# Kernel tuning notes

Measured on AMD Instinct MI355X. Metric: run time of the kernel, lower is better.

## Reference

```python
import jax, jax.numpy as jnp
import numpy as np
from jax import lax

B, N, D = 8, 16384, 64
NPOINT, NSAMPLE, RADIUS = 1024, 32, 0.1
MLP = [3 + D, 64, 64, 128]
BN_EPS = 1e-5


def setup_inputs() -> dict:
    key = jax.random.key(0)
    ks = jax.random.split(key, 8)
    inp = {
        'xyz': jax.random.uniform(ks[0], (B, 3, N), dtype=jnp.float32),
        'points': jax.random.normal(ks[1], (B, D, N), dtype=jnp.float32),
    }
    for i, (cin, cout) in enumerate(zip(MLP[:-1], MLP[1:]), start=1):
        inp[f'w{i}'] = jax.random.normal(ks[1 + i], (cout, cin), dtype=jnp.float32) / np.sqrt(cin)
        inp[f'b{i}'] = jnp.zeros((cout,), jnp.float32)
        inp[f'g{i}'] = jnp.ones((cout,), jnp.float32)
        inp[f'be{i}'] = jnp.zeros((cout,), jnp.float32)
    return inp


def farthest_point_sample(xyz, npoint):
    # xyz: (B, N, 3). Deterministic start at index 0 (torch uses randint).
    b, n, _ = xyz.shape

    def step(carry, _):
        distance, farthest = carry  # (B,N), (B,)
        centroid = jnp.take_along_axis(xyz, farthest[:, None, None], axis=1)  # (B,1,3)
        dist = jnp.sum((xyz - centroid) ** 2, axis=-1)  # (B,N)
        distance = jnp.minimum(distance, dist)
        new_far = jnp.argmax(distance, axis=-1).astype(jnp.int32)
        return (distance, new_far), farthest

    init = (jnp.full((b, n), 1e10, xyz.dtype), jnp.zeros((b,), jnp.int32))
    _, idxs = lax.scan(step, init, None, length=npoint)  # (npoint, B)
    return idxs.T  # (B, npoint)


def query_ball_point(radius, nsample, xyz, new_xyz):
    # xyz: (B,N,3), new_xyz: (B,S,3) -> (B,S,nsample) int32
    b, n, _ = xyz.shape
    # squared pairwise distances (B,S,N)
    sqr = (jnp.sum(new_xyz ** 2, -1)[:, :, None]
           + jnp.sum(xyz ** 2, -1)[:, None, :]
           - 2.0 * jnp.einsum('bsc,bnc->bsn', new_xyz, xyz))
    group_idx = jnp.where(sqr > radius ** 2, n, jnp.arange(n, dtype=jnp.int32))
    group_idx = jnp.sort(group_idx, axis=-1)[:, :, :nsample]
    first = group_idx[:, :, :1]
    return jnp.where(group_idx == n, first, group_idx)


def reference(xyz, points, w1, b1, g1, be1, w2, b2, g2, be2, w3, b3, g3, be3):
    xyz_t = xyz.transpose(0, 2, 1)      # (B,N,3)
    pts_t = points.transpose(0, 2, 1)   # (B,N,D)
    bsz = xyz_t.shape[0]

    fps_idx = farthest_point_sample(xyz_t, NPOINT)          # (B,S)
    bidx2 = jnp.arange(bsz)[:, None]
    new_xyz = xyz_t[bidx2, fps_idx]                          # (B,S,3)

    idx = query_ball_point(RADIUS, NSAMPLE, xyz_t, new_xyz)  # (B,S,ns)
    bidx3 = jnp.arange(bsz)[:, None, None]
    grouped_xyz = xyz_t[bidx3, idx] - new_xyz[:, :, None, :]  # (B,S,ns,3)
    grouped_pts = pts_t[bidx3, idx]                           # (B,S,ns,D)
    feat = jnp.concatenate([grouped_xyz, grouped_pts], axis=-1)  # (B,S,ns,C)

    for w, b, g, be in ((w1, b1, g1, be1), (w2, b2, g2, be2), (w3, b3, g3, be3)):
        feat = jnp.einsum('bsnc,oc->bsno', feat, w) + b
        mean = feat.mean(axis=(0, 1, 2))
        var = feat.var(axis=(0, 1, 2))  # biased, as torch BN uses for normalization
        feat = (feat - mean) * lax.rsqrt(var + BN_EPS) * g + be
        feat = jax.nn.relu(feat)

    new_points = feat.max(axis=2)  # max over nsample -> (B,S,Cout)
    return new_xyz.transpose(0, 2, 1), new_points.transpose(0, 2, 1)
```

## Files before the change

kernel.cpp:

```cpp
#include <hip/hip_runtime.h>
#include <hip/hip_bf16.h>
#include <stdint.h>

#define BATCH 8
#define NPTS  16384
#define DIMF  64
#define SPTS  1024
#define NSAMP 32
#define MTOT  (BATCH*SPTS*NSAMP)
#define CELLS 512

__device__ __forceinline__ float bfu_lo(uint32_t u){ return __uint_as_float(u<<16); }
__device__ __forceinline__ float bfu_hi(uint32_t u){ return __uint_as_float(u & 0xffff0000u); }
__device__ __forceinline__ uint16_t f2bf(float f){
  __hip_bfloat16 h = __float2bfloat16(f);
  uint16_t u; __builtin_memcpy(&u, &h, 2); return u;
}

__device__ __forceinline__ unsigned long long shfl_xor_u64(unsigned long long v, int off){
  unsigned lo = (unsigned)v, hi = (unsigned)(v>>32);
  lo = __shfl_xor(lo, off); hi = __shfl_xor(hi, off);
  return ((unsigned long long)hi<<32) | lo;
}

__global__ __launch_bounds__(256) void transpose_kernel(const float* __restrict__ pts,
                                                        float* __restrict__ ptsT){
  __shared__ float tile[32][33];
  int b = blockIdx.z;
  int n0 = blockIdx.x*32, c0 = blockIdx.y*32;
  int tx = threadIdx.x & 31, ty = threadIdx.x >> 5;
  const float* src = pts + (size_t)b*DIMF*NPTS;
  float* dst = ptsT + (size_t)b*NPTS*DIMF;
#pragma unroll
  for (int j=0;j<4;j++)
    tile[ty+8*j][tx] = src[(size_t)(c0+ty+8*j)*NPTS + n0 + tx];
  __syncthreads();
#pragma unroll
  for (int j=0;j<4;j++)
    dst[(size_t)(n0+ty+8*j)*DIMF + c0 + tx] = tile[tx][ty+8*j];
}

__device__ __forceinline__ int cell_of(float x, float y, float z){
  int ix=(int)(x*8.0f); ix = ix<0?0:(ix>7?7:ix);
  int iy=(int)(y*8.0f); iy = iy<0?0:(iy>7?7:iy);
  int iz=(int)(z*8.0f); iz = iz<0?0:(iz>7?7:iz);
  return (ix<<6)|(iy<<3)|iz;
}

__global__ __launch_bounds__(512) void fps_kernel(const float* __restrict__ xyz,
                                                  float* __restrict__ out0,
                                                  float4* __restrict__ sortg){
  int b = blockIdx.x;
  const float* X = xyz + (size_t)b*3*NPTS;
  float4* sp = sortg + (size_t)b*NPTS;
  int t = threadIdx.x, lane = t & 63, w = t >> 6;

  __shared__ float dst_s[NPTS];
  __shared__ int   hist[CELLS];
  __shared__ int   cursor[CELLS];
  __shared__ int   cstart[CELLS+1];
  __shared__ float cmaxv[CELLS];
  __shared__ int   cmaxk[CELLS];
  __shared__ float cwx[CELLS], cwy[CELLS], cwz[CELLS];
  __shared__ int   wsum[8];
  __shared__ float4 pf4[2][8];
  __shared__ unsigned long long pk64[2][8];

  if (t < CELLS) hist[t] = 0;
  __syncthreads();
#pragma unroll
  for (int k=0;k<32;k++){
    int n = t + (k<<9);
    atomicAdd(&hist[cell_of(X[n],X[NPTS+n],X[2*NPTS+n])],1);
  }
  __syncthreads();
  {
    int v = hist[t], inc = v;
#pragma unroll
    for (int off=1; off<64; off<<=1){ int u=__shfl_up(inc,off); if(lane>=off) inc+=u; }
    if (lane==63) wsum[w] = inc;
    __syncthreads();
    if (t==0){ int acc=0; for(int i=0;i<8;i++){int x=wsum[i]; wsum[i]=acc; acc+=x;} }
    __syncthreads();
    int ex = inc - v + wsum[w];
    cstart[t]=ex; cursor[t]=ex;
    cmaxv[t] = (v>0)?1e10f:0.0f;
    cmaxk[t] = 16383;
    if (t==0) cstart[CELLS]=NPTS;
  }
  __syncthreads();
#pragma unroll
  for (int k=0;k<32;k++){
    int n = t + (k<<9);
    float x=X[n], y=X[NPTS+n], z=X[2*NPTS+n];
    int c = cell_of(x,y,z);
    int pos = atomicAdd(&cursor[c],1);
    sp[pos] = make_float4(x,y,z,__int_as_float(n));
  }
  for (int n=t;n<NPTS;n+=512) dst_s[n]=1e10f;
  __syncthreads();

  int ix = (((lane>>5)&1)<<2) | (((lane>>4)&1)<<1) | ((w>>2)&1);
  int iy = (((lane>>3)&1)<<2) | (((lane>>2)&1)<<1) | ((w>>1)&1);
  int iz = (((lane>>1)&1)<<2) | (( lane    &1)<<1) | ( w    &1);
  int cm = (ix<<6)|(iy<<3)|iz;
  float lox=ix*0.125f, loy=iy*0.125f, loz=iz*0.125f;

  float cx=X[0], cy=X[NPTS], cz=X[2*NPTS];
  float* o = out0 + (size_t)b*3*SPTS;
  for (int s=0;s<SPTS;s++){
    if (t==0){ o[s]=cx; o[SPTS+s]=cy; o[2*SPTS+s]=cz; }
    if (s==SPTS-1) break;
    float dxx = fmaxf(fmaxf(lox-cx, cx-(lox+0.125f)),0.f);
    float dyy = fmaxf(fmaxf(loy-cy, cy-(loy+0.125f)),0.f);
    float dzz = fmaxf(fmaxf(loz-cz, cz-(loz+0.125f)),0.f);
    float lb = dxx*dxx+dyy*dyy+dzz*dzz;
    bool dirty = (lb*(1.0f-4e-6f)-4e-6f) < cmaxv[cm];
    unsigned long long mask = __ballot(dirty);
    while (mask){
      int l = (int)__builtin_ctzll(mask); mask &= mask-1;
      int jx = (((l>>5)&1)<<2) | (((l>>4)&1)<<1) | ((w>>2)&1);
      int jy = (((l>>3)&1)<<2) | (((l>>2)&1)<<1) | ((w>>1)&1);
      int jz = (((l>>1)&1)<<2) | (( l    &1)<<1) | ( w    &1);
      int c = (jx<<6)|(jy<<3)|jz;
      int st = cstart[c], en = cstart[c+1];
      if (st >= en) continue;
      unsigned long long bp = 0ull; float bd=0.f,bx=0.f,by=0.f,bz=0.f;
      for (int base=st; base<en; base+=64){
        int pos = base+lane;
        if (pos<en){
          float4 pq = sp[pos];
          float ddx=__fsub_rn(pq.x,cx), ddy=__fsub_rn(pq.y,cy), ddz=__fsub_rn(pq.z,cz);
          float d = __fadd_rn(__fadd_rn(__fmul_rn(ddx,ddx),__fmul_rn(ddy,ddy)),
                              __fmul_rn(ddz,ddz));
          float od = dst_s[pos];
          d = fminf(od, d);
          dst_s[pos] = d;
          int orig = __float_as_int(pq.w);
          unsigned long long pk =
            ((unsigned long long)__float_as_uint(d)<<32) | (unsigned)(16383-orig);
          if (pk > bp){ bp=pk; bd=d; bx=pq.x; by=pq.y; bz=pq.z; }
        }
      }
      unsigned long long rp = bp;
#pragma unroll
      for (int off=1; off<64; off<<=1){
        unsigned long long op = shfl_xor_u64(rp, off);
        rp = (op>rp)? op : rp;
      }
      unsigned long long wm = __ballot(bp==rp);
      int wl = (int)__builtin_ctzll(wm);
      if (lane==wl){
        cmaxv[c]=bd;
        cmaxk[c]=16383-(int)(bp & 0xffffffffull);
        cwx[c]=bx; cwy[c]=by; cwz[c]=bz;
      }
    }
    __builtin_amdgcn_wave_barrier();
    int p = s & 1;
    {
      float v = cmaxv[cm]; int kk = cmaxk[cm];
      unsigned long long p2 =
        ((unsigned long long)__float_as_uint(v)<<32) | (unsigned)(16383-kk);
      unsigned long long r2 = p2;
#pragma unroll
      for (int off=1; off<64; off<<=1){
        unsigned long long o2 = shfl_xor_u64(r2, off);
        r2 = (o2>r2)? o2 : r2;
      }
      unsigned long long wm2 = __ballot(p2==r2);
      int wl2 = (int)__builtin_ctzll(wm2);
      if (lane==wl2){
        pf4[p][w] = make_float4(cwx[cm], cwy[cm], cwz[cm], 0.f);
        pk64[p][w] = r2;
      }
    }
    __syncthreads();
    {
      unsigned long long fv = pk64[p][lane&7], fr = fv;
#pragma unroll
      for (int off=1; off<8; off<<=1){
        unsigned long long of = shfl_xor_u64(fr, off);
        fr = (of>fr)? of : fr;
      }
      unsigned long long fm = __ballot(fv==fr);
      int fl = (int)__builtin_ctzll(fm) & 7;
      float4 cc = pf4[p][fl];
      cx=cc.x; cy=cc.y; cz=cc.z;
    }
  }
}

__global__ __launch_bounds__(256) void ball_kernel(const float* __restrict__ xyz,
                                                   const float* __restrict__ newxyz,
                                                   int* __restrict__ idxo){
  int b  = blockIdx.x >> 5;
  int sc = blockIdx.x & 31;
  const float* X  = xyz + (size_t)b*3*NPTS;
  int t = threadIdx.x, lane = t & 63, w = t >> 6;
  __shared__ float lx[512], ly[512], lz[512], ls[512];
  __shared__ int done;
  if (t==0) done = 0;
  const float rsq = 0.01f;
  float nx[8], ny[8], nz[8], sn[8];
  int cnt[8], first[8];
  int sbase = sc*32 + w*8;
#pragma unroll
  for (int q=0;q<8;q++){
    int s = sbase + q;
    nx[q] = newxyz[(size_t)b*3*SPTS + s];
    ny[q] = newxyz[(size_t)b*3*SPTS + SPTS + s];
    nz[q] = newxyz[(size_t)b*3*SPTS + 2*SPTS + s];
    sn[q] = __fadd_rn(__fadd_rn(__fmul_rn(nx[q],nx[q]),__fmul_rn(ny[q],ny[q])),
                      __fmul_rn(nz[q],nz[q]));
    cnt[q]=0; first[q]=0;
  }
  __syncthreads();
  for (int T=0;T<32;T++){
    {
      float ax = X[T*512 + t], ay = X[NPTS + T*512 + t], az = X[2*NPTS + T*512 + t];
      lx[t]=ax; ly[t]=ay; lz[t]=az;
      ls[t] = __fadd_rn(__fadd_rn(__fmul_rn(ax,ax),__fmul_rn(ay,ay)),__fmul_rn(az,az));
      float bx = X[T*512 + t + 256], by = X[NPTS + T*512 + t + 256], bz = X[2*NPTS + T*512 + t + 256];
      lx[t+256]=bx; ly[t+256]=by; lz[t+256]=bz;
      ls[t+256] = __fadd_rn(__fadd_rn(__fmul_rn(bx,bx),__fmul_rn(by,by)),__fmul_rn(bz,bz));
    }
    __syncthreads();
#pragma unroll
    for (int q=0;q<8;q++){
      if (cnt[q] >= NSAMP) continue;
      int s = sbase + q;
      int* op = idxo + ((size_t)(b*SPTS + s))*NSAMP;
      for (int c=0;c<8;c++){
        int li = c*64 + lane;
        float dot = fmaf(nz[q], lz[li], fmaf(ny[q], ly[li], __fmul_rn(nx[q], lx[li])));
        float sq  = __fsub_rn(__fadd_rn(sn[q], ls[li]), __fmul_rn(2.0f, dot));
        bool in = (sq <= rsq);
        unsigned long long m = __ballot(in);
        if (cnt[q]==0 && m) first[q] = T*512 + c*64 + (int)__builtin_ctzll(m);
        if (in){
          int slot = cnt[q] + (int)__popcll(m & ((1ull<<lane)-1ull));
          if (slot < NSAMP) op[slot] = T*512 + li;
        }
        cnt[q] += (int)__popcll(m);
        if (cnt[q] >= NSAMP){ if (lane==0) atomicAdd(&done,1); break; }
      }
    }
    __syncthreads();
    if (done >= 32) break;
  }
#pragma unroll
  for (int q=0;q<8;q++){
    if (cnt[q] < NSAMP){
      int s = sbase + q;
      int* op = idxo + ((size_t)(b*SPTS + s))*NSAMP;
      if (lane >= cnt[q] && lane < NSAMP) op[lane] = first[q];
    }
  }
}

__global__ __launch_bounds__(256) void gemm1_kernel(const float* __restrict__ xyz,
                                                    const float* __restrict__ ptsT,
                                                    const int* __restrict__ idx,
                                                    const float* __restrict__ newxyz,
                                                    const float* __restrict__ w1,
                                                    const float* __restrict__ b1,
                                                    uint16_t* __restrict__ y1){
  __shared__ float As[128*69];
  __shared__ float Ws[67*64];
  __shared__ float bias[64];
  __shared__ int   ndx[128];
  __shared__ float nxs[4][3];
  int t = threadIdx.x;
  int g0 = blockIdx.x*128;
  if (t < 128) ndx[t] = idx[g0 + t];
  if (t < 12){
    int grp = t/3, c = t%3;
    int bs = (g0>>5) + grp; int b = bs>>10, s = bs & 1023;
    nxs[grp][c] = newxyz[(size_t)b*3*SPTS + c*SPTS + s];
  }
  if (t < 64) bias[t] = b1[t];
  for (int e=t; e<67*64; e+=256){ int k=e>>6, c=e&63; Ws[k*64+c] = w1[c*67+k]; }
  __syncthreads();
  {
    int r = t>>1, h = t&1;
    int n = ndx[r];
    int bs = (g0>>5) + (r>>5); int b = bs>>10;
    const float* pr = ptsT + ((size_t)(b*NPTS + n))*64 + h*32;
    float* ar = As + r*69;
    if (h==0){
      int grp = r>>5;
      ar[0] = __fsub_rn(xyz[(size_t)b*3*NPTS + n],          nxs[grp][0]);
      ar[1] = __fsub_rn(xyz[(size_t)b*3*NPTS + NPTS + n],   nxs[grp][1]);
      ar[2] = __fsub_rn(xyz[(size_t)b*3*NPTS + 2*NPTS + n], nxs[grp][2]);
    }
    float* ap = ar + 3 + h*32;
#pragma unroll
    for (int j=0;j<8;j++){
      float4 v = *(const float4*)(pr + j*4);
      ap[j*4+0]=v.x; ap[j*4+1]=v.y; ap[j*4+2]=v.z; ap[j*4+3]=v.w;
    }
  }
  __syncthreads();
  int rg = t>>3, cg = t&7;
  float acc[4][8];
#pragma unroll
  for (int i=0;i<4;i++)
#pragma unroll
    for (int j=0;j<8;j++) acc[i][j]=0.f;
  for (int k=0;k<67;k++){
    float a0 = As[(rg*4+0)*69+k];
    float a1 = As[(rg*4+1)*69+k];
    float a2 = As[(rg*4+2)*69+k];
    float a3 = As[(rg*4+3)*69+k];
    const float* wr = Ws + k*64 + cg*8;
    float4 w0 = *(const float4*)wr;
    float4 w1v = *(const float4*)(wr+4);
    float wj[8] = {w0.x,w0.y,w0.z,w0.w,w1v.x,w1v.y,w1v.z,w1v.w};
#pragma unroll
    for (int j=0;j<8;j++){
      acc[0][j] = fmaf(a0, wj[j], acc[0][j]);
      acc[1][j] = fmaf(a1, wj[j], acc[1][j]);
      acc[2][j] = fmaf(a2, wj[j], acc[2][j]);
      acc[3][j] = fmaf(a3, wj[j], acc[3][j]);
    }
  }
#pragma unroll
  for (int i=0;i<4;i++){
    int gr = g0 + rg*4 + i;
    uint16_t* yr = y1 + (size_t)gr*64 + cg*8;
    uint4 vv;
    uint32_t u[4];
#pragma unroll
    for (int j=0;j<4;j++){
      float v0 = acc[i][2*j]   + bias[cg*8+2*j];
      float v1 = acc[i][2*j+1] + bias[cg*8+2*j+1];
      u[j] = (uint32_t)f2bf(v0) | ((uint32_t)f2bf(v1)<<16);
    }
    vv.x=u[0]; vv.y=u[1]; vv.z=u[2]; vv.w=u[3];
    *(uint4*)yr = vv;
  }
}

__global__ __launch_bounds__(256) void gemm2_kernel(const uint16_t* __restrict__ yin,
                                                    const float* __restrict__ w2,
                                                    const float* __restrict__ b2,
                                                    const float* __restrict__ scale,
                                                    const float* __restrict__ shift,
                                                    uint16_t* __restrict__ yout){
  __shared__ float As[128*65];
  __shared__ float Ws[64*64];
  __shared__ float bias[64], sc[64], sh[64];
  int t = threadIdx.x;
  int g0 = blockIdx.x*128;
  if (t < 64){ bias[t]=b2[t]; sc[t]=scale[t]; sh[t]=shift[t]; }
  for (int e=t; e<64*64; e+=256){ int k=e>>6, c=e&63; Ws[k*64+c] = w2[c*64+k]; }
  __syncthreads();
  {
    int r = t>>1, h = t&1;
    const uint4* yv = (const uint4*)(yin + (size_t)(g0+r)*64 + h*32);
    float* ar = As + r*65 + h*32;
#pragma unroll
    for (int j=0;j<4;j++){
      uint4 u = yv[j];
      uint32_t vv[4] = {u.x,u.y,u.z,u.w};
#pragma unroll
      for (int m=0;m<4;m++){
        int c = h*32 + j*8 + m*2;
        ar[j*8+m*2]   = fmaxf(fmaf(bfu_lo(vv[m]), sc[c],   sh[c]),   0.f);
        ar[j*8+m*2+1] = fmaxf(fmaf(bfu_hi(vv[m]), sc[c+1], sh[c+1]), 0.f);
      }
    }
  }
  __syncthreads();
  int rg = t>>3, cg = t&7;
  float acc[4][8];
#pragma unroll
  for (int i=0;i<4;i++)
#pragma unroll
    for (int j=0;j<8;j++) acc[i][j]=0.f;
  for (int k=0;k<64;k++){
    float a0 = As[(rg*4+0)*65+k];
    float a1 = As[(rg*4+1)*65+k];
    float a2 = As[(rg*4+2)*65+k];
    float a3 = As[(rg*4+3)*65+k];
    const float* wr = Ws + k*64 + cg*8;
    float4 w0 = *(const float4*)wr;
    float4 w1v = *(const float4*)(wr+4);
    float wj[8] = {w0.x,w0.y,w0.z,w0.w,w1v.x,w1v.y,w1v.z,w1v.w};
#pragma unroll
    for (int j=0;j<8;j++){
      acc[0][j] = fmaf(a0, wj[j], acc[0][j]);
      acc[1][j] = fmaf(a1, wj[j], acc[1][j]);
      acc[2][j] = fmaf(a2, wj[j], acc[2][j]);
      acc[3][j] = fmaf(a3, wj[j], acc[3][j]);
    }
  }
#pragma unroll
  for (int i=0;i<4;i++){
    int gr = g0 + rg*4 + i;
    uint16_t* yr = yout + (size_t)gr*64 + cg*8;
    uint4 vv; uint32_t u[4];
#pragma unroll
    for (int j=0;j<4;j++){
      float v0 = acc[i][2*j]   + bias[cg*8+2*j];
      float v1 = acc[i][2*j+1] + bias[cg*8+2*j+1];
      u[j] = (uint32_t)f2bf(v0) | ((uint32_t)f2bf(v1)<<16);
    }
    vv.x=u[0]; vv.y=u[1]; vv.z=u[2]; vv.w=u[3];
    *(uint4*)yr = vv;
  }
}

__global__ __launch_bounds__(256) void gemm3_kernel(const uint16_t* __restrict__ yin,
                                                    const float* __restrict__ w3,
                                                    const float* __restrict__ b3,
                                                    const float* __restrict__ scale,
                                                    const float* __restrict__ shift,
                                                    uint16_t* __restrict__ yout){
  __shared__ float As[64*65];
  __shared__ float Ws[64*128];
  __shared__ float bias[128], sc[64], sh[64];
  int t = threadIdx.x;
  int g0 = blockIdx.x*64;
  if (t < 128) bias[t]=b3[t];
  if (t < 64){ sc[t]=scale[t]; sh[t]=shift[t]; }
  for (int e=t; e<64*128; e+=256){ int k=e>>7, c=e&127; Ws[k*128+c] = w3[c*64+k]; }
  __syncthreads();
  {
    int r = t>>2, h = t&3;
    const uint4* yv = (const uint4*)(yin + (size_t)(g0+r)*64 + h*16);
    float* ar = As + r*65 + h*16;
#pragma unroll
    for (int j=0;j<2;j++){
      uint4 u = yv[j];
      uint32_t vv[4] = {u.x,u.y,u.z,u.w};
#pragma unroll
      for (int m=0;m<4;m++){
        int c = h*16 + j*8 + m*2;
        ar[j*8+m*2]   = fmaxf(fmaf(bfu_lo(vv[m]), sc[c],   sh[c]),   0.f);
        ar[j*8+m*2+1] = fmaxf(fmaf(bfu_hi(vv[m]), sc[c+1], sh[c+1]), 0.f);
      }
    }
  }
  __syncthreads();
  int rg = t>>4, cg = t&15;
  float acc[4][8];
#pragma unroll
  for (int i=0;i<4;i++)
#pragma unroll
    for (int j=0;j<8;j++) acc[i][j]=0.f;
  for (int k=0;k<64;k++){
    float a0 = As[(rg*4+0)*65+k];
    float a1 = As[(rg*4+1)*65+k];
    float a2 = As[(rg*4+2)*65+k];
    float a3 = As[(rg*4+3)*65+k];
    const float* wr = Ws + k*128 + cg*8;
    float4 w0 = *(const float4*)wr;
    float4 w1v = *(const float4*)(wr+4);
    float wj[8] = {w0.x,w0.y,w0.z,w0.w,w1v.x,w1v.y,w1v.z,w1v.w};
#pragma unroll
    for (int j=0;j<8;j++){
      acc[0][j] = fmaf(a0, wj[j], acc[0][j]);
      acc[1][j] = fmaf(a1, wj[j], acc[1][j]);
      acc[2][j] = fmaf(a2, wj[j], acc[2][j]);
      acc[3][j] = fmaf(a3, wj[j], acc[3][j]);
    }
  }
#pragma unroll
  for (int i=0;i<4;i++){
    int gr = g0 + rg*4 + i;
    uint16_t* yr = yout + (size_t)gr*128 + cg*8;
    uint4 vv; uint32_t u[4];
#pragma unroll
    for (int j=0;j<4;j++){
      float v0 = acc[i][2*j]   + bias[cg*8+2*j];
      float v1 = acc[i][2*j+1] + bias[cg*8+2*j+1];
      u[j] = (uint32_t)f2bf(v0) | ((uint32_t)f2bf(v1)<<16);
    }
    vv.x=u[0]; vv.y=u[1]; vv.z=u[2]; vv.w=u[3];
    *(uint4*)yr = vv;
  }
}

template<int C>
__global__ __launch_bounds__(256) void stats_kernel(const uint16_t* __restrict__ y,
                                                    float* __restrict__ gsum,
                                                    float* __restrict__ gsq){
  constexpr int CP  = C/2;
  constexpr int RSL = 256/CP;
  int t = threadIdx.x;
  int c0 = t % CP, rs = t / CP;
  float s0=0.f,q0=0.f,s1=0.f,q1=0.f;
#pragma unroll 4
  for (int i=0;i<512/RSL;i++){
    int r = blockIdx.x*512 + rs + i*RSL;
    uint32_t u = *(const uint32_t*)(y + (size_t)r*C + 2*c0);
    float v0 = bfu_lo(u), v1 = bfu_hi(u);
    s0 += v0; q0 += v0*v0; s1 += v1; q1 += v1*v1;
  }
  __shared__ float red[4][256];
  red[0][t]=s0; red[1][t]=q0; red[2][t]=s1; red[3][t]=q1;
  __syncthreads();
  if (t < CP){
    float a0=0,a1=0,a2=0,a3=0;
    for (int k=0;k<RSL;k++){
      a0+=red[0][k*CP+t]; a1+=red[1][k*CP+t]; a2+=red[2][k*CP+t]; a3+=red[3][k*CP+t];
    }
    atomicAdd(&gsum[2*t],   a0); atomicAdd(&gsq[2*t],   a1);
    atomicAdd(&gsum[2*t+1], a2); atomicAdd(&gsq[2*t+1], a3);
  }
}

__global__ void finalize_kernel(const float* __restrict__ gsum, const float* __restrict__ gsq,
                                const float* __restrict__ g, const float* __restrict__ be,
                                float* __restrict__ scale, float* __restrict__ shift, int C){
  int c = threadIdx.x;
  if (c >= C) return;
  double mean = (double)gsum[c] / (double)MTOT;
  double var  = (double)gsq[c] / (double)MTOT - mean*mean;
  double s    = (double)g[c] / sqrt(var + 1e-5);
  scale[c] = (float)s;
  shift[c] = (float)((double)be[c] - mean*s);
}

__global__ __launch_bounds__(256) void maxpool_kernel(const uint16_t* __restrict__ y3,
                                                      const float* __restrict__ scale,
                                                      const float* __restrict__ shift,
                                                      float* __restrict__ out1){
  __shared__ float tr[16][129];
  int t = threadIdx.x;
  int b = blockIdx.x >> 6;
  int s0 = (blockIdx.x & 63) * 16;
  int ch = t & 127, sl0 = t >> 7;
  float scv = scale[ch], shv = shift[ch];
  for (int sl=sl0; sl<16; sl+=2){
    int bs = b*SPTS + s0 + sl;
    const uint16_t* yr = y3 + (size_t)bs*NSAMP*128 + ch;
    float m = 0.0f;
#pragma unroll 4
    for (int k=0;k<NSAMP;k++){
      float v = __uint_as_float(((uint32_t)yr[k*128])<<16);
      float z = fmaxf(fmaf(v, scv, shv), 0.f);
      m = fmaxf(m, z);
    }
    tr[sl][ch] = m;
  }
  __syncthreads();
  int ch2 = t >> 1, hh = t & 1;
  float vals[8];
#pragma unroll
  for (int i=0;i<8;i++) vals[i] = tr[hh*8+i][ch2];
  float* op = out1 + (size_t)b*131072 + (size_t)ch2*1024 + s0 + hh*8;
  float4 v0; v0.x=vals[0]; v0.y=vals[1]; v0.z=vals[2]; v0.w=vals[3];
  float4 v1; v1.x=vals[4]; v1.y=vals[5]; v1.z=vals[6]; v1.w=vals[7];
  *(float4*)op = v0;
  *(float4*)(op+4) = v1;
}

extern "C" void kernel_launch(void* const* d_in, const int* in_sizes, int n_in,
                              void* d_out, int out_size, void* d_ws, size_t ws_size,
                              hipStream_t stream){
  (void)in_sizes; (void)n_in; (void)out_size; (void)ws_size;
  const float* xyz = (const float*)d_in[0];
  const float* pts = (const float*)d_in[1];
  const float* w1 = (const float*)d_in[2];  const float* b1 = (const float*)d_in[3];
  const float* g1 = (const float*)d_in[4];  const float* be1 = (const float*)d_in[5];
  const float* w2 = (const float*)d_in[6];  const float* b2 = (const float*)d_in[7];
  const float* g2 = (const float*)d_in[8];  const float* be2 = (const float*)d_in[9];
  const float* w3 = (const float*)d_in[10]; const float* b3 = (const float*)d_in[11];
  const float* g3 = (const float*)d_in[12]; const float* be3 = (const float*)d_in[13];

  float* out0 = (float*)d_out;
  float* out1 = out0 + BATCH*3*SPTS;

  char* ws = (char*)d_ws;
  float*    ptsT = (float*)(ws + 0);
  int*      idx  = (int*)  (ws + 34078720);
  uint16_t* y1   = (uint16_t*)(ws + 35127296);
  uint16_t* y2   = (uint16_t*)(ws + 68681728);
  uint16_t* y3   = (uint16_t*)(ws + 102236160);
  float*    stats = (float*)(ws + 169345024);
  float4* sortg = (float4*)(ws + 35127296);
  float* gsum1 = stats;        float* gsq1 = stats + 128;
  float* gsum2 = stats + 256;  float* gsq2 = stats + 384;
  float* gsum3 = stats + 512;  float* gsq3 = stats + 640;
  float* scale1 = stats + 768; float* shift1 = stats + 896;
  float* scale2 = stats + 1024; float* shift2 = stats + 1152;
  float* scale3 = stats + 1280; float* shift3 = stats + 1408;

  hipMemsetAsync(stats, 0, 768*sizeof(float), stream);

  transpose_kernel<<<dim3(NPTS/32, DIMF/32, BATCH), 256, 0, stream>>>(pts, ptsT);
  fps_kernel<<<BATCH, 512, 0, stream>>>(xyz, out0, sortg);
  ball_kernel<<<BATCH*32, 256, 0, stream>>>(xyz, out0, idx);
  gemm1_kernel<<<MTOT/128, 256, 0, stream>>>(xyz, ptsT, idx, out0, w1, b1, y1);
  stats_kernel<64><<<512, 256, 0, stream>>>(y1, gsum1, gsq1);
  finalize_kernel<<<1, 128, 0, stream>>>(gsum1, gsq1, g1, be1, scale1, shift1, 64);
  gemm2_kernel<<<MTOT/128, 256, 0, stream>>>(y1, w2, b2, scale1, shift1, y2);
  stats_kernel<64><<<512, 256, 0, stream>>>(y2, gsum2, gsq2);
  finalize_kernel<<<1, 128, 0, stream>>>(gsum2, gsq2, g2, be2, scale2, shift2, 64);
  gemm3_kernel<<<MTOT/64, 256, 0, stream>>>(y2, w3, b3, scale2, shift2, y3);
  stats_kernel<128><<<512, 256, 0, stream>>>(y3, gsum3, gsq3);
  finalize_kernel<<<1, 128, 0, stream>>>(gsum3, gsq3, g3, be3, scale3, shift3, 128);
  maxpool_kernel<<<BATCH*(SPTS/16), 256, 0, stream>>>(y3, scale3, shift3, out1);
}
```

Measured before the change: 3.225 ms.

## Run FPS iteration loop in a single wavefront with register-resident cell maxima

After the spatial bucketing, the farthest-point-sampling loop now runs on one 64-lane wave instead of eight waves. Each lane keeps the per-cell maximum, its packed index and its coordinates for eight cells in registers. This removes the per-iteration __syncthreads and the shared-memory cross-wave reduction. The first iteration is done per lane serially over its cells. The cost is less parallelism when rescanning dirty cells, since one wave now walks all dirty cells serially, and more register pressure.

```diff
diff --git a/kernel.cpp b/kernel.cpp
--- a/kernel.cpp
+++ b/kernel.cpp
@@ -59,12 +59,7 @@
   __shared__ int   hist[CELLS];
   __shared__ int   cursor[CELLS];
   __shared__ int   cstart[CELLS+1];
-  __shared__ float cmaxv[CELLS];
-  __shared__ int   cmaxk[CELLS];
-  __shared__ float cwx[CELLS], cwy[CELLS], cwz[CELLS];
   __shared__ int   wsum[8];
-  __shared__ float4 pf4[2][8];
-  __shared__ unsigned long long pk64[2][8];
 
   if (t < CELLS) hist[t] = 0;
   __syncthreads();
@@ -84,8 +79,6 @@
     __syncthreads();
     int ex = inc - v + wsum[w];
     cstart[t]=ex; cursor[t]=ex;
-    cmaxv[t] = (v>0)?1e10f:0.0f;
-    cmaxk[t] = 16383;
     if (t==0) cstart[CELLS]=NPTS;
   }
   __syncthreads();
@@ -97,96 +90,94 @@
     int pos = atomicAdd(&cursor[c],1);
     sp[pos] = make_float4(x,y,z,__int_as_float(n));
   }
-  for (int n=t;n<NPTS;n+=512) dst_s[n]=1e10f;
-  __syncthreads();
-
-  int ix = (((lane>>5)&1)<<2) | (((lane>>4)&1)<<1) | ((w>>2)&1);
-  int iy = (((lane>>3)&1)<<2) | (((lane>>2)&1)<<1) | ((w>>1)&1);
-  int iz = (((lane>>1)&1)<<2) | (( lane    &1)<<1) | ( w    &1);
-  int cm = (ix<<6)|(iy<<3)|iz;
-  float lox=ix*0.125f, loy=iy*0.125f, loz=iz*0.125f;
+  __syncthreads();
+  if (w != 0) return;
+
+  int st[8], en[8];
+#pragma unroll
+  for (int j=0;j<8;j++){ int c=j*64+lane; st[j]=cstart[c]; en[j]=cstart[c+1]; }
+  float loy = (float)(lane>>3)*0.125f, loz = (float)(lane&7)*0.125f;
+  unsigned long long rpk[8];
+  float rx[8], ry[8], rz[8];
 
   float cx=X[0], cy=X[NPTS], cz=X[2*NPTS];
   float* o = out0 + (size_t)b*3*SPTS;
-  for (int s=0;s<SPTS;s++){
-    if (t==0){ o[s]=cx; o[SPTS+s]=cy; o[2*SPTS+s]=cz; }
+  if (lane==0){ o[0]=cx; o[SPTS]=cy; o[2*SPTS]=cz; }
+
+#pragma unroll
+  for (int j=0;j<8;j++){
+    unsigned long long bp=0ull; float bx=0.f,by=0.f,bz=0.f;
+    for (int pos=st[j]; pos<en[j]; ++pos){
+      float4 pq = sp[pos];
+      float ddx=__fsub_rn(pq.x,cx), ddy=__fsub_rn(pq.y,cy), ddz=__fsub_rn(pq.z,cz);
+      float d = __fadd_rn(__fadd_rn(__fmul_rn(ddx,ddx),__fmul_rn(ddy,ddy)),
+                          __fmul_rn(ddz,ddz));
+      dst_s[pos] = d;
+      int orig = __float_as_int(pq.w);
+      unsigned long long pk =
+        ((unsigned long long)__float_as_uint(d)<<32) | (unsigned)(16383-orig);
+      if (pk > bp){ bp=pk; bx=pq.x; by=pq.y; bz=pq.z; }
+    }
+    rpk[j]=bp; rx[j]=bx; ry[j]=by; rz[j]=bz;
+  }
+
+  for (int s=1; s<SPTS; s++){
+    unsigned long long bm=rpk[0]; float bx=rx[0], by=ry[0], bz=rz[0];
+#pragma unroll
+    for (int j=1;j<8;j++){
+      if (rpk[j] > bm){ bm=rpk[j]; bx=rx[j]; by=ry[j]; bz=rz[j]; }
+    }
+    unsigned long long rm=bm;
+#pragma unroll
+    for (int off=1; off<64; off<<=1){
+      unsigned long long om = shfl_xor_u64(rm, off);
+      rm = (om>rm)? om : rm;
+    }
+    int wl = (int)__builtin_ctzll(__ballot(bm==rm));
+    cx = __shfl(bx, wl); cy = __shfl(by, wl); cz = __shfl(bz, wl);
+    if (lane==0){ o[s]=cx; o[SPTS+s]=cy; o[2*SPTS+s]=cz; }
     if (s==SPTS-1) break;
-    float dxx = fmaxf(fmaxf(lox-cx, cx-(lox+0.125f)),0.f);
     float dyy = fmaxf(fmaxf(loy-cy, cy-(loy+0.125f)),0.f);
     float dzz = fmaxf(fmaxf(loz-cz, cz-(loz+0.125f)),0.f);
-    float lb = dxx*dxx+dyy*dyy+dzz*dzz;
-    bool dirty = (lb*(1.0f-4e-6f)-4e-6f) < cmaxv[cm];
-    unsigned long long mask = __ballot(dirty);
-    while (mask){
-      int l = (int)__builtin_ctzll(mask); mask &= mask-1;
-      int jx = (((l>>5)&1)<<2) | (((l>>4)&1)<<1) | ((w>>2)&1);
-      int jy = (((l>>3)&1)<<2) | (((l>>2)&1)<<1) | ((w>>1)&1);
-      int jz = (((l>>1)&1)<<2) | (( l    &1)<<1) | ( w    &1);
-      int c = (jx<<6)|(jy<<3)|jz;
-      int st = cstart[c], en = cstart[c+1];
-      if (st >= en) continue;
-      unsigned long long bp = 0ull; float bd=0.f,bx=0.f,by=0.f,bz=0.f;
-      for (int base=st; base<en; base+=64){
-        int pos = base+lane;
-        if (pos<en){
-          float4 pq = sp[pos];
-          float ddx=__fsub_rn(pq.x,cx), ddy=__fsub_rn(pq.y,cy), ddz=__fsub_rn(pq.z,cz);
-          float d = __fadd_rn(__fadd_rn(__fmul_rn(ddx,ddx),__fmul_rn(ddy,ddy)),
-                              __fmul_rn(ddz,ddz));
-          float od = dst_s[pos];
-          d = fminf(od, d);
-          dst_s[pos] = d;
-          int orig = __float_as_int(pq.w);
-          unsigned long long pk =
-            ((unsigned long long)__float_as_uint(d)<<32) | (unsigned)(16383-orig);
-          if (pk > bp){ bp=pk; bd=d; bx=pq.x; by=pq.y; bz=pq.z; }
+    float dyz2 = dyy*dyy + dzz*dzz;
+#pragma unroll
+    for (int j=0;j<8;j++){
+      float lox = (float)j*0.125f;
+      float dxx = fmaxf(fmaxf(lox-cx, cx-(lox+0.125f)),0.f);
+      float lb  = dxx*dxx + dyz2;
+      float cmv = __uint_as_float((unsigned)(rpk[j]>>32));
+      bool dd = (st[j]<en[j]) && ((lb*(1.0f-4e-6f)-4e-6f) < cmv);
+      unsigned long long mj = __ballot(dd);
+      while (mj){
+        int l = (int)__builtin_ctzll(mj); mj &= mj-1;
+        int cs = __shfl(st[j], l), ce = __shfl(en[j], l);
+        unsigned long long bp=0ull; float px=0.f,py=0.f,pz=0.f;
+        for (int base=cs; base<ce; base+=64){
+          int pos = base+lane;
+          if (pos < ce){
+            float4 pq = sp[pos];
+            float od = dst_s[pos];
+            float ddx=__fsub_rn(pq.x,cx), ddy=__fsub_rn(pq.y,cy), ddz=__fsub_rn(pq.z,cz);
+            float d = __fadd_rn(__fadd_rn(__fmul_rn(ddx,ddx),__fmul_rn(ddy,ddy)),
+                                __fmul_rn(ddz,ddz));
+            d = fminf(od, d);
+            dst_s[pos] = d;
+            int orig = __float_as_int(pq.w);
+            unsigned long long pk =
+              ((unsigned long long)__float_as_uint(d)<<32) | (unsigned)(16383-orig);
+            if (pk > bp){ bp=pk; px=pq.x; py=pq.y; pz=pq.z; }
+          }
         }
+        unsigned long long rp=bp;
+#pragma unroll
+        for (int off=1; off<64; off<<=1){
+          unsigned long long op = shfl_xor_u64(rp, off);
+          rp = (op>rp)? op : rp;
+        }
+        int wl2 = (int)__builtin_ctzll(__ballot(bp==rp));
+        float gx=__shfl(px,wl2), gy=__shfl(py,wl2), gz=__shfl(pz,wl2);
+        if (lane==l){ rpk[j]=rp; rx[j]=gx; ry[j]=gy; rz[j]=gz; }
       }
-      unsigned long long rp = bp;
-#pragma unroll
-      for (int off=1; off<64; off<<=1){
-        unsigned long long op = shfl_xor_u64(rp, off);
-        rp = (op>rp)? op : rp;
-      }
-      unsigned long long wm = __ballot(bp==rp);
-      int wl = (int)__builtin_ctzll(wm);
-      if (lane==wl){
-        cmaxv[c]=bd;
-        cmaxk[c]=16383-(int)(bp & 0xffffffffull);
-        cwx[c]=bx; cwy[c]=by; cwz[c]=bz;
-      }
-    }
-    __builtin_amdgcn_wave_barrier();
-    int p = s & 1;
-    {
-      float v = cmaxv[cm]; int kk = cmaxk[cm];
-      unsigned long long p2 =
-        ((unsigned long long)__float_as_uint(v)<<32) | (unsigned)(16383-kk);
-      unsigned long long r2 = p2;
-#pragma unroll
-      for (int off=1; off<64; off<<=1){
-        unsigned long long o2 = shfl_xor_u64(r2, off);
-        r2 = (o2>r2)? o2 : r2;
-      }
-      unsigned long long wm2 = __ballot(p2==r2);
-      int wl2 = (int)__builtin_ctzll(wm2);
-      if (lane==wl2){
-        pf4[p][w] = make_float4(cwx[cm], cwy[cm], cwz[cm], 0.f);
-        pk64[p][w] = r2;
-      }
-    }
-    __syncthreads();
-    {
-      unsigned long long fv = pk64[p][lane&7], fr = fv;
-#pragma unroll
-      for (int off=1; off<8; off<<=1){
-        unsigned long long of = shfl_xor_u64(fr, off);
-        fr = (of>fr)? of : fr;
-      }
-      unsigned long long fm = __ballot(fv==fr);
-      int fl = (int)__builtin_ctzll(fm) & 7;
-      float4 cc = pf4[p][fl];
-      cx=cc.x; cy=cc.y; cz=cc.z;
     }
   }
 }
```

New measurement: 10.37 ms. 3.22x slower.
